# Optimization experiments

Hardware: AMD Instinct MI355X
Metric: run time of the kernel (lower is better)

## Reference

```python
import jax, jax.numpy as jnp
import numpy as np

B, S, D = 1, 2048, 2048
H, G, HD = 32, 8, 64          # heads, kv groups, head_dim
GS = H // G                   # group size = 4
EPS = 1e-6


def _rmsnorm(v, w):
    vf = v.astype(jnp.float32)
    n = vf * jax.lax.rsqrt(jnp.mean(vf * vf, axis=-1, keepdims=True) + EPS)
    return (n * (1.0 + w.astype(jnp.float32))).astype(v.dtype)


def _rope(v, cos, sin):
    # v: [b, h, s, hd]; cos/sin: [s, hd] (rot_dim == head_dim)
    half = v.shape[-1] // 2
    x1, x2 = v[..., :half], v[..., half:]
    rotated = jnp.concatenate([-x2, x1], axis=-1)
    c = cos[None, None, :, :]
    s = sin[None, None, :, :]
    return (v * c + rotated * s).astype(v.dtype)


def setup_inputs() -> dict:
    key = jax.random.key(0)
    ks = jax.random.split(key, 8)
    x = jax.random.normal(ks[0], (B, S, D), dtype=jnp.float32)
    # causal mask: True above diagonal => masked out
    mask = jnp.triu(jnp.ones((S, S), dtype=bool), k=1)
    # standard RoPE tables, full rotary dim == head_dim
    inv_freq = 1.0 / (10000.0 ** (jnp.arange(0, HD, 2, dtype=jnp.float32) / HD))
    angles = jnp.arange(S, dtype=jnp.float32)[:, None] * inv_freq[None, :]
    angles = jnp.concatenate([angles, angles], axis=-1)  # [S, HD]
    cos = jnp.cos(angles)
    sin = jnp.sin(angles)
    sc = 1.0 / np.sqrt(D)
    Wq = jax.random.normal(ks[1], (2 * H * HD, D), dtype=jnp.float32) * sc
    Wk = jax.random.normal(ks[2], (G * HD, D), dtype=jnp.float32) * sc
    Wv = jax.random.normal(ks[3], (G * HD, D), dtype=jnp.float32) * sc
    Wo = jax.random.normal(ks[4], (D, H * HD), dtype=jnp.float32) * sc
    q_norm_w = jnp.zeros((HD,), dtype=jnp.float32)
    k_norm_w = jnp.zeros((HD,), dtype=jnp.float32)
    return {"x": x, "mask": mask, "cos": cos, "sin": sin, "Wq": Wq,
            "Wk": Wk, "Wv": Wv, "Wo": Wo,
            "q_norm_w": q_norm_w, "k_norm_w": k_norm_w}


def reference(x, mask, cos, sin, Wq, Wk, Wv, Wo, q_norm_w, k_norm_w):
    b, s, _ = x.shape
    d_out = H * HD
    # fused q + gate projection: [b, s, H, 2*HD]
    qg = jnp.einsum('bsd,ed->bse', x, Wq).reshape(b, s, H, 2 * HD)
    q = qg[..., :HD]                         # [b, s, H, HD]
    gate = qg[..., HD:].reshape(b, s, d_out)  # [b, s, d_out]
    k = jnp.einsum('bsd,ed->bse', x, Wk).reshape(b, s, G, HD)
    v = jnp.einsum('bsd,ed->bse', x, Wv).reshape(b, s, G, HD)
    q = q.transpose(0, 2, 1, 3)   # [b, H, s, HD]
    k = k.transpose(0, 2, 1, 3)   # [b, G, s, HD]
    v = v.transpose(0, 2, 1, 3)
    q = _rmsnorm(q, q_norm_w)
    k = _rmsnorm(k, k_norm_w)
    q = _rope(q, cos[:s], sin[:s])
    k = _rope(k, cos[:s], sin[:s])
    # GQA without materializing repeated K/V: group queries as [b, G, GS, s, HD]
    qg_ = q.reshape(b, G, GS, s, HD)
    scores = jnp.einsum('bghqd,bgkd->bghqk', qg_, k)   # [b, G, GS, s, s]
    scores = jnp.where(mask[None, None, None, :s, :s], -jnp.inf, scores)
    scale = HD ** (-0.5)
    w = jax.nn.softmax((scores * scale).astype(jnp.float32), axis=-1).astype(q.dtype)
    ctx = jnp.einsum('bghqk,bgkd->bghqd', w, v)        # [b, G, GS, s, HD]
    ctx = ctx.reshape(b, H, s, HD).transpose(0, 2, 1, 3).reshape(b, s, d_out)
    ctx = ctx * jax.nn.sigmoid(gate)
    return jnp.einsum('bse,de->bsd', ctx, Wo)
```

## Files before the change

### kernel.cpp

```cpp
#include <hip/hip_runtime.h>

typedef __bf16 bf16;
typedef __bf16 bf16x4 __attribute__((ext_vector_type(4)));
typedef __bf16 bf16x8 __attribute__((ext_vector_type(8)));
typedef float f32x4 __attribute__((ext_vector_type(4)));

#define DEV static __device__ __forceinline__

constexpr int S  = 2048;
constexpr int D  = 2048;
constexpr int H  = 32;
constexpr int G  = 8;
constexpr int HD = 64;
constexpr int NQG = 2 * H * HD;
constexpr int NKV = G * HD;
constexpr int LDP = 72;

DEV bf16x8 load8(const bf16* p) { return *reinterpret_cast<const bf16x8*>(p); }

DEV f32x4 mfma16(bf16x8 a, bf16x8 b, f32x4 c) {
  return __builtin_amdgcn_mfma_f32_16x16x32_bf16(a, b, c, 0, 0, 0);
}

DEV void gload_lds16(const bf16* g, bf16* l) {
  __builtin_amdgcn_global_load_lds(
      (const __attribute__((address_space(1))) void*)g,
      (__attribute__((address_space(3))) void*)l, 16, 0, 0);
}

template <int NISS>
DEV void stage_tile(bf16* lds, const bf16* src_row0, size_t ld, int k0, int tid) {
  const int w = tid >> 6, l = tid & 63;
#pragma unroll
  for (int i = 0; i < NISS; ++i) {
    int blk = w * NISS + i;
    int r = blk * 8 + (l >> 3);
    int c = (l & 7) ^ (r & 7);
    gload_lds16(src_row0 + (size_t)r * ld + k0 + c * 8, lds + blk * 512);
  }
}

DEV bf16x8 fragr(const bf16* T, int row, int chunk) {
  return load8(T + row * 64 + (((chunk ^ (row & 7)) << 3)));
}

DEV float fexp2(float x) { return __builtin_amdgcn_exp2f(x); }
DEV float frcp(float x)  { return __builtin_amdgcn_rcpf(x); }

__global__ __launch_bounds__(256) void cvt_f32_bf16(
    const float* __restrict__ in, bf16* __restrict__ out, int n)
{
  int i = (int)(blockIdx.x * 256u + threadIdx.x) * 8;
  if (i >= n) return;
  const float4* p = reinterpret_cast<const float4*>(in + i);
  float4 a = p[0], b = p[1];
  bf16x8 o;
  o[0] = (bf16)a.x; o[1] = (bf16)a.y; o[2] = (bf16)a.z; o[3] = (bf16)a.w;
  o[4] = (bf16)b.x; o[5] = (bf16)b.y; o[6] = (bf16)b.z; o[7] = (bf16)b.w;
  *reinterpret_cast<bf16x8*>(out + i) = o;
}

__global__ __launch_bounds__(256, 3) void gemm_qkv(
    const bf16* __restrict__ X, const bf16* __restrict__ Wq,
    const bf16* __restrict__ Wk, const bf16* __restrict__ Wv,
    bf16* __restrict__ qg, bf16* __restrict__ kpre, bf16* __restrict__ vt)
{
  __shared__ __align__(16) bf16 As[128 * 64];
  __shared__ __align__(16) bf16 Bs[128 * 64];

  const int tid  = threadIdx.x;
  const int wave = tid >> 6;
  const int lane = tid & 63;
  const int ln = lane & 15, hi = lane >> 4;
  const int wm = wave >> 1, wn = wave & 1;
  const int m0 = blockIdx.y * 128;
  const int nt = blockIdx.x;

  const bf16* W; int n0;
  if (nt < 32)      { W = Wq; n0 = nt * 128; }
  else if (nt < 36) { W = Wk; n0 = (nt - 32) * 128; }
  else              { W = Wv; n0 = (nt - 36) * 128; }

  const bf16* arow = X + (size_t)m0 * D;
  const bf16* brow = W + (size_t)n0 * D;

  f32x4 acc[4][4] = {};

  for (int k0 = 0; k0 < D; k0 += 64) {
    __syncthreads();
    stage_tile<4>(As, arow, D, k0, tid);
    stage_tile<4>(Bs, brow, D, k0, tid);
    __syncthreads();
#pragma unroll
    for (int kk = 0; kk < 64; kk += 32) {
      bf16x8 a[4], b[4];
#pragma unroll
      for (int mi = 0; mi < 4; ++mi) a[mi] = fragr(As, wm * 64 + mi * 16 + ln, (kk >> 3) + hi);
#pragma unroll
      for (int ni = 0; ni < 4; ++ni) b[ni] = fragr(Bs, wn * 64 + ni * 16 + ln, (kk >> 3) + hi);
#pragma unroll
      for (int mi = 0; mi < 4; ++mi)
#pragma unroll
        for (int ni = 0; ni < 4; ++ni)
          acc[mi][ni] = mfma16(a[mi], b[ni], acc[mi][ni]);
    }
  }

  if (nt < 36) {
    bf16* C; int ldc;
    if (nt < 32) { C = qg; ldc = NQG; } else { C = kpre; ldc = NKV; }
#pragma unroll
    for (int mi = 0; mi < 4; ++mi)
#pragma unroll
      for (int ni = 0; ni < 4; ++ni)
#pragma unroll
        for (int j = 0; j < 4; ++j) {
          int r = m0 + wm * 64 + mi * 16 + hi * 4 + j;
          int c = n0 + wn * 64 + ni * 16 + ln;
          C[(size_t)r * ldc + c] = (bf16)acc[mi][ni][j];
        }
  } else {
    int nrel = (nt - 36) * 128;
#pragma unroll
    for (int mi = 0; mi < 4; ++mi)
#pragma unroll
      for (int ni = 0; ni < 4; ++ni)
#pragma unroll
        for (int j = 0; j < 4; ++j) {
          int r = m0 + wm * 64 + mi * 16 + hi * 4 + j;
          int c = nrel + wn * 64 + ni * 16 + ln;
          vt[(size_t)c * S + r] = (bf16)acc[mi][ni][j];
        }
  }
}

__global__ __launch_bounds__(256, 3) void gemm_out(
    const bf16* __restrict__ A, const bf16* __restrict__ W,
    float* __restrict__ C)
{
  __shared__ __align__(16) bf16 As[128 * 64];
  __shared__ __align__(16) bf16 Bs[64 * 64];

  const int tid  = threadIdx.x;
  const int wave = tid >> 6;
  const int lane = tid & 63;
  const int ln = lane & 15, hi = lane >> 4;
  const int m0 = blockIdx.y * 128;
  const int n0 = blockIdx.x * 64;

  const bf16* arow = A + (size_t)m0 * D;
  const bf16* brow = W + (size_t)n0 * D;

  f32x4 acc[2][4] = {};

  for (int k0 = 0; k0 < D; k0 += 64) {
    __syncthreads();
    stage_tile<4>(As, arow, D, k0, tid);
    stage_tile<2>(Bs, brow, D, k0, tid);
    __syncthreads();
#pragma unroll
    for (int kk = 0; kk < 64; kk += 32) {
      bf16x8 a[2], b[4];
#pragma unroll
      for (int mi = 0; mi < 2; ++mi) a[mi] = fragr(As, wave * 32 + mi * 16 + ln, (kk >> 3) + hi);
#pragma unroll
      for (int ni = 0; ni < 4; ++ni) b[ni] = fragr(Bs, ni * 16 + ln, (kk >> 3) + hi);
#pragma unroll
      for (int mi = 0; mi < 2; ++mi)
#pragma unroll
        for (int ni = 0; ni < 4; ++ni)
          acc[mi][ni] = mfma16(a[mi], b[ni], acc[mi][ni]);
    }
  }

#pragma unroll
  for (int mi = 0; mi < 2; ++mi)
#pragma unroll
    for (int ni = 0; ni < 4; ++ni)
#pragma unroll
      for (int j = 0; j < 4; ++j) {
        int r = m0 + wave * 32 + mi * 16 + hi * 4 + j;
        int c = n0 + ni * 16 + ln;
        C[(size_t)r * D + c] = acc[mi][ni][j];
      }
}

__global__ __launch_bounds__(256) void rmsrope(
    const bf16* __restrict__ qg, const bf16* __restrict__ kpre,
    const float* __restrict__ cosb, const float* __restrict__ sinb,
    const float* __restrict__ qw, const float* __restrict__ kw,
    bf16* __restrict__ qrot, bf16* __restrict__ krot)
{
  int wid  = (int)((blockIdx.x * (unsigned)blockDim.x + threadIdx.x) >> 6);
  int lane = threadIdx.x & 63;
  int s  = wid & (S - 1);
  int hh = wid >> 11;

  float v, wgt;
  if (hh < H) { v = (float)qg[(size_t)s * NQG + hh * 128 + lane];        wgt = qw[lane]; }
  else        { v = (float)kpre[(size_t)s * NKV + (hh - H) * 64 + lane]; wgt = kw[lane]; }

  float ss = v * v;
#pragma unroll
  for (int m = 1; m < 64; m <<= 1) ss += __shfl_xor(ss, m);
  float xf = v * (1.0f / sqrtf(ss * (1.0f / 64.0f) + 1e-6f)) * (1.0f + wgt);

  float part = __shfl_xor(xf, 32);
  float rot  = (lane < 32) ? -part : part;
  float c  = cosb[(size_t)s * HD + lane];
  float sn = sinb[(size_t)s * HD + lane];
  float r  = xf * c + rot * sn;

  if (hh < H) {
    qrot[((size_t)hh * S + s) * HD + lane] = (bf16)(r * 0.18033688011111204f);
  } else {
    krot[((size_t)(hh - H) * S + s) * HD + lane] = (bf16)r;
  }
}

#define BARRIER() asm volatile("s_barrier" ::: "memory")
#define VMDRAIN() asm volatile("s_waitcnt vmcnt(0)" ::: "memory")

DEV void attn_phase(const bf16* __restrict__ qrot, const bf16* __restrict__ krow,
                    const bf16* __restrict__ vrow, const bf16* __restrict__ qg,
                    bf16* __restrict__ ctxg,
                    bf16* Kb0, bf16* Kb1, bf16* Vb0, bf16* Vb1, bf16* pw,
                    int h, int qchunk, int nt, int ln, int hi, int tid)
{
  const int qb = qchunk * 64 + (tid >> 6) * 16;
  const int q  = qb + ln;

  const bf16* qbase = qrot + ((size_t)h * S + qb + ln) * HD + hi * 8;
  bf16x8 q0 = load8(qbase);
  bf16x8 q1 = load8(qbase + 32);

  f32x4 po[4] = {};
  float m = -INFINITY, l = 0.f;

  stage_tile<2>(Kb0, krow, 64, 0, tid);
  stage_tile<2>(Vb0, vrow, S, 0, tid);
  VMDRAIN();
  BARRIER();

  int cur = 0;
  for (int t = 0; t < nt; ++t) {
    const bf16* Kb = cur ? Kb1 : Kb0;
    const bf16* Vb = cur ? Vb1 : Vb0;

    if (t + 1 < nt) {
      bf16* Kn = cur ? Kb0 : Kb1;
      bf16* Vn = cur ? Vb0 : Vb1;
      stage_tile<2>(Kn, krow + (size_t)(t + 1) * 64 * 64, 64, 0, tid);
      stage_tile<2>(Vn, vrow, S, (t + 1) * 64, tid);
    }

    bf16x8 kf0[4], kf1[4];
#pragma unroll
    for (int kr = 0; kr < 4; ++kr) {
      kf0[kr] = fragr(Kb, kr * 16 + ln, hi);
      kf1[kr] = fragr(Kb, kr * 16 + ln, hi + 4);
    }
    bf16x8 bv0[4], bv1[4];
#pragma unroll
    for (int dt = 0; dt < 4; ++dt) {
      bv0[dt] = fragr(Vb, dt * 16 + ln, hi);
      bv1[dt] = fragr(Vb, dt * 16 + ln, hi + 4);
    }

    f32x4 sc[4] = {};
    __builtin_amdgcn_s_setprio(1);
#pragma unroll
    for (int kr = 0; kr < 4; ++kr) {
      sc[kr] = mfma16(kf0[kr], q0, sc[kr]);
      sc[kr] = mfma16(kf1[kr], q1, sc[kr]);
    }
    __builtin_amdgcn_s_setprio(0);

    float pmax = -INFINITY;
    if (t == nt - 1) {
      const int key0 = t << 6;
#pragma unroll
      for (int kr = 0; kr < 4; ++kr)
#pragma unroll
        for (int j = 0; j < 4; ++j) {
          int key = key0 + kr * 16 + hi * 4 + j;
          float v = (key <= q) ? sc[kr][j] : -INFINITY;
          sc[kr][j] = v;
          pmax = fmaxf(pmax, v);
        }
    } else {
#pragma unroll
      for (int kr = 0; kr < 4; ++kr)
#pragma unroll
        for (int j = 0; j < 4; ++j) pmax = fmaxf(pmax, sc[kr][j]);
    }
    pmax = fmaxf(pmax, __shfl_xor(pmax, 16));
    pmax = fmaxf(pmax, __shfl_xor(pmax, 32));

    if (__any(pmax > m + 8.0f)) {
      float mn = fmaxf(m, pmax);
      float c  = fexp2(m - mn);
      l *= c;
      float cc[4];
#pragma unroll
      for (int j = 0; j < 4; ++j) cc[j] = __shfl(c, hi * 4 + j);
#pragma unroll
      for (int dt = 0; dt < 4; ++dt)
#pragma unroll
        for (int j = 0; j < 4; ++j) po[dt][j] *= cc[j];
      m = mn;
    }

    float ps = 0.f;
#pragma unroll
    for (int kr = 0; kr < 4; ++kr)
#pragma unroll
      for (int j = 0; j < 4; ++j) {
        float e = fexp2(sc[kr][j] - m);
        sc[kr][j] = e;
        ps += e;
      }
    ps += __shfl_xor(ps, 16);
    ps += __shfl_xor(ps, 32);
    l += ps;

#pragma unroll
    for (int kr = 0; kr < 4; ++kr) {
      unsigned w0, w1;
      asm("v_cvt_pk_bf16_f32 %0, %1, %2" : "=v"(w0) : "v"(sc[kr][0]), "v"(sc[kr][1]));
      asm("v_cvt_pk_bf16_f32 %0, %1, %2" : "=v"(w1) : "v"(sc[kr][2]), "v"(sc[kr][3]));
      uint2 w = {w0, w1};
      *reinterpret_cast<uint2*>(pw + ln * LDP + kr * 16 + hi * 4) = w;
    }
    bf16x8 pa0 = load8(pw + ln * LDP + hi * 8);
    bf16x8 pa1 = load8(pw + ln * LDP + 32 + hi * 8);

    __builtin_amdgcn_s_setprio(1);
#pragma unroll
    for (int dt = 0; dt < 4; ++dt) {
      po[dt] = mfma16(pa0, bv0[dt], po[dt]);
      po[dt] = mfma16(pa1, bv1[dt], po[dt]);
    }
    __builtin_amdgcn_s_setprio(0);

    VMDRAIN();
    BARRIER();
    cur ^= 1;
  }

  float lf[4];
#pragma unroll
  for (int j = 0; j < 4; ++j) lf[j] = __shfl(l, hi * 4 + j);
#pragma unroll
  for (int dt = 0; dt < 4; ++dt)
#pragma unroll
    for (int j = 0; j < 4; ++j) {
      int qq = qb + hi * 4 + j;
      int d  = dt * 16 + ln;
      float o  = po[dt][j] * frcp(lf[j]);
      float gv = (float)qg[(size_t)qq * NQG + h * 128 + 64 + d];
      float sg = frcp(1.0f + fexp2(gv * -1.442695040888963f));
      ctxg[(size_t)qq * D + h * 64 + d] = (bf16)(o * sg);
    }
}

__global__ __launch_bounds__(256) void attn(
    const bf16* __restrict__ qrot, const bf16* __restrict__ krot,
    const bf16* __restrict__ vt, const bf16* __restrict__ qg,
    bf16* __restrict__ ctxg)
{
  __shared__ __align__(16) bf16 Kbuf[2][64 * 64];
  __shared__ __align__(16) bf16 Vbuf[2][64 * 64];
  __shared__ __align__(16) bf16 Pl[4][16 * LDP];

  const int tid  = threadIdx.x;
  const int lane = tid & 63;
  const int ln = lane & 15, hi = lane >> 4;

  const int bid = blockIdx.x;
  const int g   = bid & 7;
  const int i   = bid >> 3;
  const int h   = g * 4 + (i & 3);
  const int pr  = i >> 2;
  bf16* pw = &Pl[tid >> 6][0];

  const bf16* krow = krot + (size_t)g * S * HD;
  const bf16* vrow = vt + (size_t)g * 64 * S;

  attn_phase(qrot, krow, vrow, qg, ctxg,
             &Kbuf[0][0], &Kbuf[1][0], &Vbuf[0][0], &Vbuf[1][0], pw,
             h, pr, pr + 1, ln, hi, tid);
  attn_phase(qrot, krow, vrow, qg, ctxg,
             &Kbuf[0][0], &Kbuf[1][0], &Vbuf[0][0], &Vbuf[1][0], pw,
             h, 31 - pr, 32 - pr, ln, hi, tid);
}

extern "C" void kernel_launch(void* const* d_in, const int* in_sizes, int n_in,
                              void* d_out, int out_size, void* d_ws, size_t ws_size,
                              hipStream_t stream) {
  const float* x    = (const float*)d_in[0];
  const float* cosb = (const float*)d_in[2];
  const float* sinb = (const float*)d_in[3];
  const float* Wq   = (const float*)d_in[4];
  const float* Wk   = (const float*)d_in[5];
  const float* Wv   = (const float*)d_in[6];
  const float* Wo   = (const float*)d_in[7];
  const float* qw   = (const float*)d_in[8];
  const float* kw   = (const float*)d_in[9];

  char* ws = (char*)d_ws;
  bf16* xb   = (bf16*)(ws);
  bf16* Wqb  = (bf16*)(ws + ( 8u << 20));
  bf16* Wkb  = (bf16*)(ws + (24u << 20));
  bf16* Wvb  = (bf16*)(ws + (26u << 20));
  bf16* Wob  = (bf16*)(ws + (28u << 20));
  bf16* qg   = (bf16*)(ws + (36u << 20));
  bf16* kpre = (bf16*)(ws + (52u << 20));
  bf16* vt   = (bf16*)(ws + (54u << 20));
  bf16* qrot = (bf16*)(ws + (56u << 20));
  bf16* krot = (bf16*)(ws + (64u << 20));
  bf16* ctxg = (bf16*)(ws + (66u << 20));
  float* out = (float*)d_out;

  cvt_f32_bf16<<<dim3(2048), 256, 0, stream>>>(x,  xb,  S * D);
  cvt_f32_bf16<<<dim3(4096), 256, 0, stream>>>(Wq, Wqb, NQG * D);
  cvt_f32_bf16<<<dim3(512),  256, 0, stream>>>(Wk, Wkb, NKV * D);
  cvt_f32_bf16<<<dim3(512),  256, 0, stream>>>(Wv, Wvb, NKV * D);
  cvt_f32_bf16<<<dim3(2048), 256, 0, stream>>>(Wo, Wob, D * D);

  gemm_qkv<<<dim3(40, 16), 256, 0, stream>>>(xb, Wqb, Wkb, Wvb, qg, kpre, vt);
  rmsrope<<<dim3(20480), 256, 0, stream>>>(qg, kpre, cosb, sinb, qw, kw, qrot, krot);
  attn<<<dim3(512), 256, 0, stream>>>(qrot, krot, vt, qg, ctxg);
  gemm_out<<<dim3(32, 16), 256, 0, stream>>>(ctxg, Wob, out);
}
```

Measured before the change: 158.4 us.

## Share K/V tiles across two heads per attention block and merge conversion kernels

The attention kernel now runs 512 threads (8 waves) per block, and each block serves two query heads of the same KV group. The K/V tiles staged in LDS are shared by twice as many waves, which halves the redundant global K/V loads, and each wave issues one staging load instead of two. Separately, the five fp32-to-bf16 conversion launches become a single kernel that picks its source and destination by thread index, cutting launch overhead. The larger blocks halve the grid to 256 blocks, which may lower occupancy flexibility and load balance.

```diff
diff --git a/kernel.cpp b/kernel.cpp
--- a/kernel.cpp
+++ b/kernel.cpp
@@ -40,6 +40,13 @@
   }
 }
 
+DEV void stage64_8w(bf16* lds, const bf16* src_row0, size_t ld, int k0, int tid) {
+  const int w = tid >> 6, l = tid & 63;
+  int r = w * 8 + (l >> 3);
+  int c = (l & 7) ^ (r & 7);
+  gload_lds16(src_row0 + (size_t)r * ld + k0 + c * 8, lds + w * 512);
+}
+
 DEV bf16x8 fragr(const bf16* T, int row, int chunk) {
   return load8(T + row * 64 + (((chunk ^ (row & 7)) << 3)));
 }
@@ -47,17 +54,27 @@
 DEV float fexp2(float x) { return __builtin_amdgcn_exp2f(x); }
 DEV float frcp(float x)  { return __builtin_amdgcn_rcpf(x); }
 
-__global__ __launch_bounds__(256) void cvt_f32_bf16(
-    const float* __restrict__ in, bf16* __restrict__ out, int n)
-{
-  int i = (int)(blockIdx.x * 256u + threadIdx.x) * 8;
-  if (i >= n) return;
-  const float4* p = reinterpret_cast<const float4*>(in + i);
+__global__ __launch_bounds__(256) void cvt_all(
+    const float* __restrict__ x,  const float* __restrict__ wq,
+    const float* __restrict__ wk, const float* __restrict__ wv,
+    const float* __restrict__ wo,
+    bf16* __restrict__ xb,  bf16* __restrict__ wqb, bf16* __restrict__ wkb,
+    bf16* __restrict__ wvb, bf16* __restrict__ wob)
+{
+  long c = (long)blockIdx.x * 256 + threadIdx.x;
+  const float* src; bf16* dst; long off;
+  if      (c <  524288) { src = x;  dst = xb;  off = c; }
+  else if (c < 1572864) { src = wq; dst = wqb; off = c -  524288; }
+  else if (c < 1703936) { src = wk; dst = wkb; off = c - 1572864; }
+  else if (c < 1835008) { src = wv; dst = wvb; off = c - 1703936; }
+  else                  { src = wo; dst = wob; off = c - 1835008; }
+  long i = off * 8;
+  const float4* p = reinterpret_cast<const float4*>(src + i);
   float4 a = p[0], b = p[1];
   bf16x8 o;
   o[0] = (bf16)a.x; o[1] = (bf16)a.y; o[2] = (bf16)a.z; o[3] = (bf16)a.w;
   o[4] = (bf16)b.x; o[5] = (bf16)b.y; o[6] = (bf16)b.z; o[7] = (bf16)b.w;
-  *reinterpret_cast<bf16x8*>(out + i) = o;
+  *reinterpret_cast<bf16x8*>(dst + i) = o;
 }
 
 __global__ __launch_bounds__(256, 3) void gemm_qkv(
@@ -227,7 +244,7 @@
                     bf16* Kb0, bf16* Kb1, bf16* Vb0, bf16* Vb1, bf16* pw,
                     int h, int qchunk, int nt, int ln, int hi, int tid)
 {
-  const int qb = qchunk * 64 + (tid >> 6) * 16;
+  const int qb = qchunk * 64 + ((tid >> 6) & 3) * 16;
   const int q  = qb + ln;
 
   const bf16* qbase = qrot + ((size_t)h * S + qb + ln) * HD + hi * 8;
@@ -237,8 +254,8 @@
   f32x4 po[4] = {};
   float m = -INFINITY, l = 0.f;
 
-  stage_tile<2>(Kb0, krow, 64, 0, tid);
-  stage_tile<2>(Vb0, vrow, S, 0, tid);
+  stage64_8w(Kb0, krow, 64, 0, tid);
+  stage64_8w(Vb0, vrow, S, 0, tid);
   VMDRAIN();
   BARRIER();
 
@@ -250,8 +267,8 @@
     if (t + 1 < nt) {
       bf16* Kn = cur ? Kb0 : Kb1;
       bf16* Vn = cur ? Vb0 : Vb1;
-      stage_tile<2>(Kn, krow + (size_t)(t + 1) * 64 * 64, 64, 0, tid);
-      stage_tile<2>(Vn, vrow, S, (t + 1) * 64, tid);
+      stage64_8w(Kn, krow + (size_t)(t + 1) * 64 * 64, 64, 0, tid);
+      stage64_8w(Vn, vrow, S, (t + 1) * 64, tid);
     }
 
     bf16x8 kf0[4], kf1[4];
@@ -364,14 +381,14 @@
     }
 }
 
-__global__ __launch_bounds__(256) void attn(
+__global__ __launch_bounds__(512) void attn(
     const bf16* __restrict__ qrot, const bf16* __restrict__ krot,
     const bf16* __restrict__ vt, const bf16* __restrict__ qg,
     bf16* __restrict__ ctxg)
 {
   __shared__ __align__(16) bf16 Kbuf[2][64 * 64];
   __shared__ __align__(16) bf16 Vbuf[2][64 * 64];
-  __shared__ __align__(16) bf16 Pl[4][16 * LDP];
+  __shared__ __align__(16) bf16 Pl[8][16 * LDP];
 
   const int tid  = threadIdx.x;
   const int lane = tid & 63;
@@ -380,8 +397,9 @@
   const int bid = blockIdx.x;
   const int g   = bid & 7;
   const int i   = bid >> 3;
-  const int h   = g * 4 + (i & 3);
-  const int pr  = i >> 2;
+  const int hp  = i & 1;
+  const int pr  = i >> 1;
+  const int h   = g * 4 + hp * 2 + ((tid >> 6) >> 2);
   bf16* pw = &Pl[tid >> 6][0];
 
   const bf16* krow = krot + (size_t)g * S * HD;
@@ -422,14 +440,11 @@
   bf16* ctxg = (bf16*)(ws + (66u << 20));
   float* out = (float*)d_out;
 
-  cvt_f32_bf16<<<dim3(2048), 256, 0, stream>>>(x,  xb,  S * D);
-  cvt_f32_bf16<<<dim3(4096), 256, 0, stream>>>(Wq, Wqb, NQG * D);
-  cvt_f32_bf16<<<dim3(512),  256, 0, stream>>>(Wk, Wkb, NKV * D);
-  cvt_f32_bf16<<<dim3(512),  256, 0, stream>>>(Wv, Wvb, NKV * D);
-  cvt_f32_bf16<<<dim3(2048), 256, 0, stream>>>(Wo, Wob, D * D);
+  cvt_all<<<dim3(9216), 256, 0, stream>>>(x, Wq, Wk, Wv, Wo,
+                                          xb, Wqb, Wkb, Wvb, Wob);
 
   gemm_qkv<<<dim3(40, 16), 256, 0, stream>>>(xb, Wqb, Wkb, Wvb, qg, kpre, vt);
   rmsrope<<<dim3(20480), 256, 0, stream>>>(qg, kpre, cosb, sinb, qw, kw, qrot, krot);
-  attn<<<dim3(512), 256, 0, stream>>>(qrot, krot, vt, qg, ctxg);
+  attn<<<dim3(256), 512, 0, stream>>>(qrot, krot, vt, qg, ctxg);
   gemm_out<<<dim3(32, 16), 256, 0, stream>>>(ctxg, Wob, out);
 }
```

Measured after the change: 146.1 us. 1.08x faster.
